# Performance work log

Hardware: AMD Instinct MI355X
Metric: run time of the kernel (lower is better)

## Reference

```python
import jax, jax.numpy as jnp
import numpy as np

B, T, D, K = 16, 4096, 512, 128
ALPHA_MIN = 1e-06
OMEGA_MAX = float(np.pi)
SN_EPS = 1e-06


def setup_inputs() -> dict:
    key = jax.random.key(0)
    ks = jax.random.split(key, 7)
    x = jax.random.normal(ks[0], (B, T, D), jnp.float32)
    # irregular positive step sizes, mean ~ 1/T like the uniform-grid default
    dt = jax.random.uniform(ks[1], (B, T), jnp.float32, minval=0.1, maxval=1.9) * (1.0 / T)
    # replicate reset_parameters: target_alpha ~ U(0.01, 0.2), raw = log(expm1(alpha - alpha_min))
    target_alpha = jax.random.uniform(ks[2], (K,), jnp.float32, minval=0.01, maxval=0.2)
    s_real_raw = jnp.log(jnp.expm1(jnp.maximum(target_alpha - ALPHA_MIN, 1e-08)))
    s_imag = jax.random.uniform(ks[3], (K,), jnp.float32, minval=-np.pi, maxval=np.pi)
    # kaiming-uniform-ish proj weight [K, D] and bias [K]
    W = jax.random.normal(ks[4], (K, D), jnp.float32) * (1.0 / np.sqrt(D))
    bound = 1.0 / np.sqrt(D)
    bias = jax.random.uniform(ks[5], (K,), jnp.float32, minval=-bound, maxval=bound)
    b_log = jnp.zeros((K,), jnp.float32)  # torch stores [1,1,K]; broadcasting is identical
    u_sn = jax.random.normal(ks[6], (K,), jnp.float32)  # spectral-norm power-iteration vector
    return {"x": x, "dt": dt, "s_real_raw": s_real_raw, "s_imag": s_imag,
            "W": W, "bias": bias, "b_log": b_log, "u_sn": u_sn}


def _spectral_normalize(W, u):
    # one power iteration, u/v detached (as torch.nn.utils.spectral_norm does)
    v = W.T @ u
    v = v / (jnp.linalg.norm(v) + SN_EPS)
    u2 = W @ v
    u2 = u2 / (jnp.linalg.norm(u2) + SN_EPS)
    u2 = jax.lax.stop_gradient(u2)
    v = jax.lax.stop_gradient(v)
    sigma = u2 @ (W @ v)
    return W / sigma


def reference(x, dt, s_real_raw, s_imag, W, bias, b_log, u_sn):
    # x: [B,T,D], dt: [B,T] -> lap_feats [B,T,2K]
    alpha = jax.nn.softplus(s_real_raw) + ALPHA_MIN          # [K] strictly positive decay
    omega = jnp.clip(s_imag, -OMEGA_MAX, OMEGA_MAX)          # [K]
    Wsn = _spectral_normalize(W, u_sn)
    u = jnp.einsum('btd,kd->btk', x, Wsn) + bias             # spectral-norm projection
    dt3 = dt[..., None]                                      # [B,T,1]
    rho = jnp.exp(-alpha * dt3)                              # [B,T,K]
    theta = omega * dt3
    cos_t, sin_t = jnp.cos(theta), jnp.sin(theta)
    b_gain = jnp.exp(b_log)                                  # [K]
    inj = (1.0 - rho) * (b_gain * u)                         # [B,T,K]

    def step(carry, inp):
        c, s = carry
        r, ct, st, it = inp
        c_new = r * (c * ct - s * st) + it
        s_new = r * (c * st + s * ct) + it
        return (c_new, s_new), (c_new, s_new)

    seq = (jnp.moveaxis(rho, 1, 0), jnp.moveaxis(cos_t, 1, 0),
           jnp.moveaxis(sin_t, 1, 0), jnp.moveaxis(inj, 1, 0))  # each [T,B,K]
    init = (jnp.zeros((x.shape[0], K), x.dtype), jnp.zeros((x.shape[0], K), x.dtype))
    _, (C, S) = jax.lax.scan(step, init, seq)
    C = jnp.moveaxis(C, 0, 1)  # [B,T,K]
    S = jnp.moveaxis(S, 0, 1)
    return jnp.concatenate([C, S], axis=-1)
```

## Files before the change

kernel.cpp:

```cpp
#include <hip/hip_runtime.h>
#include <stdint.h>

#define BB 16
#define TT 4096
#define DDIM 512
#define KK 128
#define TCB 128
#define NCB (TT / TCB)
#define PI_F 3.14159265358979323846f

typedef unsigned short u16;
typedef __attribute__((ext_vector_type(8))) short short8;
typedef __attribute__((ext_vector_type(4))) float f32x4;

__device__ __forceinline__ uint32_t cvt_bf16_rn(float f) {
  uint32_t u = __float_as_uint(f);
  return (u + 0x7FFFu + ((u >> 16) & 1u)) >> 16;
}
__device__ __forceinline__ uint32_t pack2(float a, float b) {
  return cvt_bf16_rn(a) | (cvt_bf16_rn(b) << 16);
}
__device__ __forceinline__ uint4 pack8(const float4 f0, const float4 f1) {
  uint4 r;
  r.x = pack2(f0.x, f0.y);
  r.y = pack2(f0.z, f0.w);
  r.z = pack2(f1.x, f1.y);
  r.w = pack2(f1.z, f1.w);
  return r;
}
__device__ __forceinline__ void gload_lds16(const void* g, void* l) {
  __builtin_amdgcn_global_load_lds(
      (const __attribute__((address_space(1))) void*)g,
      (__attribute__((address_space(3))) void*)l, 16, 0, 0);
}
#define AT_LD(p) __hip_atomic_load((p), __ATOMIC_RELAXED, __HIP_MEMORY_SCOPE_AGENT)
#define AT_ST(p, v) __hip_atomic_store((p), (v), __ATOMIC_RELAXED, __HIP_MEMORY_SCOPE_AGENT)

__global__ __launch_bounds__(256) void k_prep(
    const float* __restrict__ W, const float* __restrict__ u_sn,
    const float* __restrict__ s_real_raw, const float* __restrict__ s_imag,
    const float* __restrict__ bias, const float* __restrict__ b_log,
    const float* __restrict__ dt,
    float* __restrict__ params, u16* __restrict__ Wp, float* __restrict__ ct) {
  int gb = blockIdx.x;
  int tid = threadIdx.x;
  if (gb < 64) {
    int idx = gb * 256 + tid;
    int k = idx >> 7;
    int d = (idx & 127) * 4;
    float4 v = *(const float4*)&W[(size_t)k * DDIM + d];
    int tile = d >> 6, dl = d & 63;
    int slot = (dl >> 3) ^ (k & 7);
    int e = dl & 7;
    size_t base = (size_t)tile * 8192 + k * 64 + slot * 8 + e;
    uint2 p;
    p.x = pack2(v.x, v.y);
    p.y = pack2(v.z, v.w);
    *(uint2*)&Wp[base] = p;
  } else if (gb < 80) {
    __shared__ float sc[256];
    int b = gb - 64;
    const float* row = dt + (size_t)b * TT;
    float* orow = ct + (size_t)b * TT;
    float loc[16];
    float s = 0.f;
    int base = tid * 16;
    for (int i = 0; i < 16; ++i) { s += row[base + i]; loc[i] = s; }
    sc[tid] = s;
    __syncthreads();
    for (int off = 1; off < 256; off <<= 1) {
      float v = (tid >= off) ? sc[tid - off] : 0.f;
      __syncthreads();
      sc[tid] += v;
      __syncthreads();
    }
    float excl = sc[tid] - s;
    for (int i = 0; i < 16; ++i) orow[base + i] = excl + loc[i];
  } else {
    __shared__ float su[KK];
    __shared__ float sv[DDIM];
    __shared__ float red[4];
    __shared__ float s_sig;
    if (tid < KK) su[tid] = u_sn[tid];
    __syncthreads();
    for (int rep = 0; rep < 2; ++rep) {
      int d = tid + rep * 256;
      float acc = 0.f;
      for (int k = 0; k < KK; ++k) acc += W[k * DDIM + d] * su[k];
      sv[d] = acc;
    }
    __syncthreads();
    float nn = 0.f;
    for (int rep = 0; rep < 2; ++rep) { float v = sv[tid + rep * 256]; nn += v * v; }
    for (int off = 32; off > 0; off >>= 1) nn += __shfl_down(nn, off, 64);
    if ((tid & 63) == 0) red[tid >> 6] = nn;
    __syncthreads();
    float vn2 = red[0] + red[1] + red[2] + red[3];
    __syncthreads();
    float vinv = 1.f / (sqrtf(vn2) + 1e-6f);
    for (int rep = 0; rep < 2; ++rep) sv[tid + rep * 256] *= vinv;
    __syncthreads();
    float wv = 0.f;
    if (tid < KK) {
      const float* wrow = W + (size_t)tid * DDIM;
      for (int d = 0; d < DDIM; ++d) wv += wrow[d] * sv[d];
    }
    float q = wv * wv;
    for (int off = 32; off > 0; off >>= 1) q += __shfl_down(q, off, 64);
    if ((tid & 63) == 0) red[tid >> 6] = q;
    __syncthreads();
    if (tid == 0) {
      float wn2 = red[0] + red[1] + red[2] + red[3];
      s_sig = wn2 / (sqrtf(wn2) + 1e-6f);
    }
    __syncthreads();
    if (tid < KK) {
      float inv_sigma = 1.f / s_sig;
      float sr = s_real_raw[tid];
      float alpha = ((sr > 20.f) ? sr : log1pf(expf(sr))) + 1e-6f;
      float om = fminf(fmaxf(s_imag[tid], -PI_F), PI_F);
      float bg = expf(b_log[tid]);
      params[tid] = alpha;
      params[KK + tid] = om;
      params[2 * KK + tid] = bg * inv_sigma;
      params[3 * KK + tid] = bg * bias[tid];
    }
  }
}

__global__ __launch_bounds__(512, 4) void k_fused(
    const float* __restrict__ x, const u16* __restrict__ Wp,
    const float* __restrict__ dt, const float* __restrict__ ct,
    const float* __restrict__ params, float* __restrict__ out,
    float* __restrict__ csum_re, float* __restrict__ csum_im,
    int* __restrict__ cnt) {
  __shared__ __align__(16) u16 smem[32768];

  const int chunk = blockIdx.x, b = blockIdx.y;
  const int tid = threadIdx.x;
  const int wv = tid >> 6, l = tid & 63;
  const int lm = l & 15, lg = l >> 4;
  const int kw = wv & 1, tw = wv >> 1;
  const int t0 = chunk * TCB;

  const int xr = tid >> 2, xq = (tid & 3) * 16;
  const size_t xbase = ((size_t)b * TT + t0 + xr) * DDIM + xq;
  const int xs0 = ((xq >> 3) ^ (xr & 7)) * 8;
  const int xs1 = (((xq >> 3) + 1) ^ (xr & 7)) * 8;

  f32x4 acc[2][4];
#pragma unroll
  for (int m = 0; m < 2; ++m)
#pragma unroll
    for (int n = 0; n < 4; ++n) acc[m][n] = (f32x4)(0.0f);

  {
    const char* wsg = (const char*)Wp + (size_t)tid * 16;
    char* wd = (char*)smem + 32768 + tid * 16;
    gload_lds16(wsg, wd);
    gload_lds16(wsg + 8192, wd + 8192);
    const float* xp = x + xbase;
    float4 f0 = *(const float4*)(xp + 0);
    float4 f1 = *(const float4*)(xp + 4);
    float4 f2 = *(const float4*)(xp + 8);
    float4 f3 = *(const float4*)(xp + 12);
    *(uint4*)&smem[xr * 64 + xs0] = pack8(f0, f1);
    *(uint4*)&smem[xr * 64 + xs1] = pack8(f2, f3);
  }
  __syncthreads();

  int cur = 0;
  for (int it = 0; it < 8; ++it) {
    float4 f0, f1, f2, f3;
    if (it < 7) {
      const float* xp = x + xbase + (it + 1) * 64;
      f0 = *(const float4*)(xp + 0);
      f1 = *(const float4*)(xp + 4);
      f2 = *(const float4*)(xp + 8);
      f3 = *(const float4*)(xp + 12);
      const char* wsg = (const char*)Wp + (size_t)(it + 1) * 16384 + tid * 16;
      char* wd = (char*)smem + 32768 + (cur ^ 1) * 16384 + tid * 16;
      gload_lds16(wsg, wd);
      gload_lds16(wsg + 8192, wd + 8192);
    }
    __builtin_amdgcn_sched_barrier(0);
    {
      const u16* xb = smem + cur * 8192;
      const u16* wb = smem + 16384 + cur * 8192;
#pragma unroll
      for (int ks = 0; ks < 2; ++ks) {
        short8 fa[2], fb[4];
#pragma unroll
        for (int m = 0; m < 2; ++m) {
          int row = tw * 32 + m * 16 + lm;
          int sw = ((ks * 4 + lg) ^ (row & 7)) * 8;
          fa[m] = *(const short8*)&xb[row * 64 + sw];
        }
#pragma unroll
        for (int n = 0; n < 4; ++n) {
          int row = kw * 64 + n * 16 + lm;
          int sw = ((ks * 4 + lg) ^ (row & 7)) * 8;
          fb[n] = *(const short8*)&wb[row * 64 + sw];
        }
#pragma unroll
        for (int m = 0; m < 2; ++m)
#pragma unroll
          for (int n = 0; n < 4; ++n)
            acc[m][n] = __builtin_amdgcn_mfma_f32_16x16x32_bf16(fa[m], fb[n], acc[m][n], 0, 0, 0);
      }
    }
    __builtin_amdgcn_sched_barrier(0);
    if (it < 7) {
      u16* xb = smem + (cur ^ 1) * 8192;
      *(uint4*)&xb[xr * 64 + xs0] = pack8(f0, f1);
      *(uint4*)&xb[xr * 64 + xs1] = pack8(f2, f3);
    }
    __syncthreads();
    cur ^= 1;
  }

  float* totr = (float*)smem;
  float* toti = (float*)smem + 512;
  float* pre_ = (float*)smem + 1024;

  float dtv[2][4], ctv[2][4];
#pragma unroll
  for (int m = 0; m < 2; ++m)
#pragma unroll
    for (int r = 0; r < 4; ++r) {
      int t = t0 + tw * 32 + m * 16 + lg * 4 + r;
      dtv[m][r] = dt[(size_t)b * TT + t];
      ctv[m][r] = ct[(size_t)b * TT + t];
    }

#pragma unroll
  for (int n = 0; n < 4; ++n) {
    int k = kw * 64 + n * 16 + lm;
    float pal = params[k], pom = params[KK + k];
    float pc1 = params[2 * KK + k], pc2 = params[3 * KK + k];
    float sr = 0.f, si2 = 0.f;
#pragma unroll
    for (int m = 0; m < 2; ++m)
#pragma unroll
      for (int r = 0; r < 4; ++r) {
        float g = acc[m][n][r];
        float a = pal * dtv[m][r];
        float omr = a * (1.f - a * (0.5f - a * (1.f / 6.f)));
        float itv = omr * (pc1 * g + pc2);
        float e = __expf(pal * ctv[m][r]);
        float sn, cs;
        __sincosf(pom * ctv[m][r], &sn, &cs);
        sr += itv * e * cs;
        si2 -= itv * e * sn;
      }
    sr += __shfl_xor(sr, 16, 64);
    sr += __shfl_xor(sr, 32, 64);
    si2 += __shfl_xor(si2, 16, 64);
    si2 += __shfl_xor(si2, 32, 64);
    if (lg == 0) { totr[tw * KK + k] = sr; toti[tw * KK + k] = si2; }
  }
  __syncthreads();
  if (tid < 256) {
    int v = tid & 127;
    float* src = (tid < 128) ? totr : toti;
    float* dst = (tid < 128) ? csum_re : csum_im;
    float tot = (src[v] + src[KK + v]) + (src[2 * KK + v] + src[3 * KK + v]);
    AT_ST(&dst[((size_t)b * NCB + chunk) * KK + v], tot);
  }
  __syncthreads();
  if (tid == 0) {
    __threadfence();
    __hip_atomic_fetch_add(&cnt[b * 64], 1, __ATOMIC_RELAXED, __HIP_MEMORY_SCOPE_AGENT);
  }

  if (chunk == 0) {
    if (tid == 0)
      while (AT_LD(&cnt[b * 64]) < NCB) __builtin_amdgcn_s_sleep(2);
    __syncthreads();
    if (tid < 256) {
      int v = tid & 127;
      float* srcp = (tid < 128) ? csum_re : csum_im;
      size_t base = (size_t)b * NCB * KK + v;
      float vals[NCB];
#pragma unroll
      for (int c = 0; c < NCB; ++c) vals[c] = AT_LD(&srcp[base + (size_t)c * KK]);
      float run = 0.f;
#pragma unroll
      for (int c = 0; c < NCB; ++c) { float t = vals[c]; AT_ST(&srcp[base + (size_t)c * KK], run); run += t; }
    }
    __syncthreads();
    if (tid == 0) {
      __threadfence();
      AT_ST(&cnt[b * 64 + 32], 1);
    }
  }
  if (tid == 0)
    while (AT_LD(&cnt[b * 64 + 32]) == 0) __builtin_amdgcn_s_sleep(2);
  __syncthreads();
  if (tid < 256) {
    int v = tid & 127;
    float* srcp = (tid < 128) ? csum_re : csum_im;
    pre_[tid] = AT_LD(&srcp[((size_t)b * NCB + chunk) * KK + v]);
  }
  __syncthreads();

#pragma unroll
  for (int n = 0; n < 4; ++n) {
    int k = kw * 64 + n * 16 + lm;
    float pal = params[k], pom = params[KK + k];
    float pc1 = params[2 * KK + k], pc2 = params[3 * KK + k];
    float cr = pre_[k], ci = pre_[KK + k];
    for (int t2 = 0; t2 < tw; ++t2) { cr += totr[t2 * KK + k]; ci += toti[t2 * KK + k]; }
#pragma unroll
    for (int m = 0; m < 2; ++m) {
      float vr[4], vi[4], e4[4], sn4[4], cs4[4];
#pragma unroll
      for (int r = 0; r < 4; ++r) {
        float g = acc[m][n][r];
        float a = pal * dtv[m][r];
        float omr = a * (1.f - a * (0.5f - a * (1.f / 6.f)));
        float itv = omr * (pc1 * g + pc2);
        float e = __expf(pal * ctv[m][r]);
        float sn, cs;
        __sincosf(pom * ctv[m][r], &sn, &cs);
        e4[r] = e; sn4[r] = sn; cs4[r] = cs;
        vr[r] = itv * e * cs;
        vi[r] = -(itv * e) * sn;
      }
      vr[1] += vr[0]; vr[2] += vr[1]; vr[3] += vr[2];
      vi[1] += vi[0]; vi[2] += vi[1]; vi[3] += vi[2];
      float ar = vr[3], ai = vi[3];
      float tr0 = ar, ti0 = ai;
      float ur = __shfl_up(ar, 16, 64);
      float ui = __shfl_up(ai, 16, 64);
      if (lg >= 1) { ar += ur; ai += ui; }
      ur = __shfl_up(ar, 32, 64);
      ui = __shfl_up(ai, 32, 64);
      if (lg >= 2) { ar += ur; ai += ui; }
      float exr = ar - tr0 + cr;
      float exi = ai - ti0 + ci;
      cr += __shfl(ar, 48 + lm, 64);
      ci += __shfl(ai, 48 + lm, 64);
#pragma unroll
      for (int r = 0; r < 4; ++r) {
        float Sre = vr[r] + exr;
        float Sim = vi[r] + exi;
        float dec = __builtin_amdgcn_rcpf(e4[r]);
        float sn = sn4[r], cs = cs4[r];
        float Rw = dec * (cs * Sre - sn * Sim);
        float Iw = dec * (cs * Sim + sn * Sre);
        size_t rowb = ((size_t)b * TT + t0 + tw * 32 + m * 16 + lg * 4 + r) * (2 * KK);
        out[rowb + k] = Rw - Iw;
        out[rowb + KK + k] = Rw + Iw;
      }
    }
  }
}

extern "C" void kernel_launch(void* const* d_in, const int* in_sizes, int n_in,
                              void* d_out, int out_size, void* d_ws, size_t ws_size,
                              hipStream_t stream) {
  const float* x    = (const float*)d_in[0];
  const float* dt   = (const float*)d_in[1];
  const float* srr  = (const float*)d_in[2];
  const float* si   = (const float*)d_in[3];
  const float* W    = (const float*)d_in[4];
  const float* bias = (const float*)d_in[5];
  const float* blog = (const float*)d_in[6];
  const float* usn  = (const float*)d_in[7];
  float* out = (float*)d_out;
  float* ws = (float*)d_ws;

  float* params  = ws;
  float* ct      = ws + 4 * KK;
  float* csum_re = ct + (size_t)BB * TT;
  float* csum_im = csum_re + (size_t)BB * NCB * KK;
  u16*   Wp      = (u16*)(csum_im + (size_t)BB * NCB * KK);
  int*   cnt     = (int*)(Wp + 65536);

  hipMemsetAsync(cnt, 0, 16 * 64 * sizeof(int), stream);
  k_prep<<<81, 256, 0, stream>>>(W, usn, srr, si, bias, blog, dt, params, Wp, ct);
  k_fused<<<dim3(NCB, BB), 512, 0, stream>>>(x, Wp, dt, ct, params, out,
                                             csum_re, csum_im, cnt);
}
```

Measured before the change: 76.41 us.

## Deepen GEMM prologue pipeline to prefetch x two stages ahead with explicit vmcnt waits

Restructures the projection GEMM main loop so x tiles are loaded two K-steps ahead into alternating register sets (xa/xb), while W tiles stream into LDS one step ahead. __syncthreads is replaced by manual s_waitcnt vmcnt/lgkmcnt and s_barrier with sched_barriers, and the loop is fully unrolled. This is meant to hide global-load latency behind the MFMA work. In exchange it uses more registers, and correctness now depends on the hand-counted vmcnt values matching the number of outstanding loads.

```diff
diff --git a/kernel.cpp b/kernel.cpp
--- a/kernel.cpp
+++ b/kernel.cpp
@@ -154,39 +154,69 @@
 #pragma unroll
     for (int n = 0; n < 4; ++n) acc[m][n] = (f32x4)(0.0f);
 
+  float4 xa[4], xb[4];
+  const char* wsrc = (const char*)Wp + (size_t)tid * 16;
+  char* wdst = (char*)smem + 32768 + tid * 16;
+
   {
-    const char* wsg = (const char*)Wp + (size_t)tid * 16;
-    char* wd = (char*)smem + 32768 + tid * 16;
-    gload_lds16(wsg, wd);
-    gload_lds16(wsg + 8192, wd + 8192);
+    gload_lds16(wsrc, wdst);
+    gload_lds16(wsrc + 8192, wdst + 8192);
     const float* xp = x + xbase;
-    float4 f0 = *(const float4*)(xp + 0);
-    float4 f1 = *(const float4*)(xp + 4);
-    float4 f2 = *(const float4*)(xp + 8);
-    float4 f3 = *(const float4*)(xp + 12);
-    *(uint4*)&smem[xr * 64 + xs0] = pack8(f0, f1);
-    *(uint4*)&smem[xr * 64 + xs1] = pack8(f2, f3);
-  }
-  __syncthreads();
-
-  int cur = 0;
-  for (int it = 0; it < 8; ++it) {
-    float4 f0, f1, f2, f3;
-    if (it < 7) {
-      const float* xp = x + xbase + (it + 1) * 64;
-      f0 = *(const float4*)(xp + 0);
-      f1 = *(const float4*)(xp + 4);
-      f2 = *(const float4*)(xp + 8);
-      f3 = *(const float4*)(xp + 12);
-      const char* wsg = (const char*)Wp + (size_t)(it + 1) * 16384 + tid * 16;
-      char* wd = (char*)smem + 32768 + (cur ^ 1) * 16384 + tid * 16;
+    xa[0] = *(const float4*)(xp + 0);
+    xa[1] = *(const float4*)(xp + 4);
+    xa[2] = *(const float4*)(xp + 8);
+    xa[3] = *(const float4*)(xp + 12);
+    __builtin_amdgcn_sched_barrier(0);
+    gload_lds16(wsrc + 16384, wdst + 16384);
+    gload_lds16(wsrc + 24576, wdst + 24576);
+    const float* xp1 = x + xbase + 64;
+    xb[0] = *(const float4*)(xp1 + 0);
+    xb[1] = *(const float4*)(xp1 + 4);
+    xb[2] = *(const float4*)(xp1 + 8);
+    xb[3] = *(const float4*)(xp1 + 12);
+    __builtin_amdgcn_sched_barrier(0);
+    asm volatile("s_waitcnt vmcnt(6)" ::: "memory");
+    __builtin_amdgcn_sched_barrier(0);
+    *(uint4*)&smem[xr * 64 + xs0] = pack8(xa[0], xa[1]);
+    *(uint4*)&smem[xr * 64 + xs1] = pack8(xa[2], xa[3]);
+    asm volatile("s_waitcnt lgkmcnt(0)" ::: "memory");
+    __builtin_amdgcn_sched_barrier(0);
+  }
+
+#pragma unroll
+  for (int j = 0; j < 8; ++j) {
+    const int p = j & 1;
+    if (j >= 1 && j <= 6) {
+      const char* wsg = (const char*)Wp + (size_t)(j + 1) * 16384 + tid * 16;
+      char* wd = (char*)smem + 32768 + ((j + 1) & 1) * 16384 + tid * 16;
       gload_lds16(wsg, wd);
       gload_lds16(wsg + 8192, wd + 8192);
     }
+    if (j <= 5) {
+      const float* xp = x + xbase + (size_t)(j + 2) * 64;
+      if (p == 0) {
+        xa[0] = *(const float4*)(xp + 0);
+        xa[1] = *(const float4*)(xp + 4);
+        xa[2] = *(const float4*)(xp + 8);
+        xa[3] = *(const float4*)(xp + 12);
+      } else {
+        xb[0] = *(const float4*)(xp + 0);
+        xb[1] = *(const float4*)(xp + 4);
+        xb[2] = *(const float4*)(xp + 8);
+        xb[3] = *(const float4*)(xp + 12);
+      }
+    }
+    __builtin_amdgcn_sched_barrier(0);
+    if (j == 0)      asm volatile("s_waitcnt vmcnt(4)" ::: "memory");
+    else if (j == 6) asm volatile("s_waitcnt vmcnt(2)" ::: "memory");
+    else if (j == 7) asm volatile("s_waitcnt vmcnt(0)" ::: "memory");
+    else             asm volatile("s_waitcnt vmcnt(6)" ::: "memory");
+    __builtin_amdgcn_sched_barrier(0);
+    __builtin_amdgcn_s_barrier();
     __builtin_amdgcn_sched_barrier(0);
     {
-      const u16* xb = smem + cur * 8192;
-      const u16* wb = smem + 16384 + cur * 8192;
+      const u16* xbuf = smem + p * 8192;
+      const u16* wbuf = smem + 16384 + p * 8192;
 #pragma unroll
       for (int ks = 0; ks < 2; ++ks) {
         short8 fa[2], fb[4];
@@ -194,13 +224,13 @@
         for (int m = 0; m < 2; ++m) {
           int row = tw * 32 + m * 16 + lm;
           int sw = ((ks * 4 + lg) ^ (row & 7)) * 8;
-          fa[m] = *(const short8*)&xb[row * 64 + sw];
+          fa[m] = *(const short8*)&xbuf[row * 64 + sw];
         }
 #pragma unroll
         for (int n = 0; n < 4; ++n) {
           int row = kw * 64 + n * 16 + lm;
           int sw = ((ks * 4 + lg) ^ (row & 7)) * 8;
-          fb[n] = *(const short8*)&wb[row * 64 + sw];
+          fb[n] = *(const short8*)&wbuf[row * 64 + sw];
         }
 #pragma unroll
         for (int m = 0; m < 2; ++m)
@@ -210,13 +240,20 @@
       }
     }
     __builtin_amdgcn_sched_barrier(0);
-    if (it < 7) {
-      u16* xb = smem + (cur ^ 1) * 8192;
-      *(uint4*)&xb[xr * 64 + xs0] = pack8(f0, f1);
-      *(uint4*)&xb[xr * 64 + xs1] = pack8(f2, f3);
-    }
-    __syncthreads();
-    cur ^= 1;
+    if (j <= 6) {
+      u16* xw = smem + (p ^ 1) * 8192;
+      if (((j + 1) & 1) == 0) {
+        *(uint4*)&xw[xr * 64 + xs0] = pack8(xa[0], xa[1]);
+        *(uint4*)&xw[xr * 64 + xs1] = pack8(xa[2], xa[3]);
+      } else {
+        *(uint4*)&xw[xr * 64 + xs0] = pack8(xb[0], xb[1]);
+        *(uint4*)&xw[xr * 64 + xs1] = pack8(xb[2], xb[3]);
+      }
+    }
+    __builtin_amdgcn_sched_barrier(0);
+    asm volatile("s_waitcnt lgkmcnt(0)" ::: "memory");
+    __builtin_amdgcn_s_barrier();
+    __builtin_amdgcn_sched_barrier(0);
   }
 
   float* totr = (float*)smem;
```

New measurement: 80.02 us. 1.05x slower.
